# Optimization experiments

Measured on AMD Instinct MI355X. Metric: run time of the kernel, lower is better.

Reference implementation:

```python
import jax, jax.numpy as jnp
import numpy as np

N_GROUPS = 32
N_HEADS = 16
EPS = 1e-5


def group_norm(x, w, b):
    # x: [B, C, T]
    B, C, T = x.shape
    xg = x.reshape(B, N_GROUPS, C // N_GROUPS, T)
    mu = xg.mean(axis=(2, 3), keepdims=True)
    var = xg.var(axis=(2, 3), keepdims=True)
    xn = ((xg - mu) * jax.lax.rsqrt(var + EPS)).reshape(B, C, T)
    return xn * w[None, :, None] + b[None, :, None]


def setup_inputs() -> dict:
    key = jax.random.key(0)
    ks = jax.random.split(key, 5)
    B, C, T = 4, 1024, 1024
    return {
        "x": jax.random.normal(ks[0], (B, C, T), jnp.float32),
        "norm_weight": jnp.ones((C,), jnp.float32),
        "norm_bias": jnp.zeros((C,), jnp.float32),
        "qkv_w": jax.random.normal(ks[1], (3 * C, C), jnp.float32) * 0.02,
        "qkv_b": jax.random.normal(ks[2], (3 * C,), jnp.float32) * 0.02,
        "proj_w": jax.random.normal(ks[3], (C, C), jnp.float32) * 0.02,
        "proj_b": jax.random.normal(ks[4], (C,), jnp.float32) * 0.02,
    }


def reference(x, norm_weight, norm_bias, qkv_w, qkv_b, proj_w, proj_b):
    B, C, T = x.shape
    H = N_HEADS
    ch = C // H
    # GroupNorm + 1x1 conv to QKV: [B, 3C, T]
    xn = group_norm(x, norm_weight, norm_bias)
    qkv = jnp.einsum('oc,bct->bot', qkv_w, xn) + qkv_b[None, :, None]
    # Legacy layout: [B, H*3*ch, T] -> [B, H, 3, ch, T]
    qkv = qkv.reshape(B, H, 3, ch, T)
    q, k, v = qkv[:, :, 0], qkv[:, :, 1], qkv[:, :, 2]
    scale = 1.0 / jnp.sqrt(jnp.sqrt(jnp.asarray(ch, x.dtype)))
    w = jnp.einsum('bhct,bhcs->bhts', q * scale, k * scale)
    w = jax.nn.softmax(w.astype(jnp.float32), axis=-1).astype(w.dtype)
    a = jnp.einsum('bhts,bhcs->bhct', w, v).reshape(B, C, T)
    h = jnp.einsum('oc,bct->bot', proj_w, a) + proj_b[None, :, None]
    return x + h
```

## Files before the change

### kernel.cpp

```cpp
#include <hip/hip_runtime.h>
#include <hip/hip_bf16.h>

typedef __bf16 bf16;
typedef bf16  bf16x4 __attribute__((ext_vector_type(4)));
typedef bf16  bf16x8 __attribute__((ext_vector_type(8)));
typedef float f32x4  __attribute__((ext_vector_type(4)));

union B8 { bf16x8 v; bf16 e[8]; };
union B4 { bf16x4 v; bf16 e[4]; };
union F4 { f32x4 v; float e[4]; };

#define GLOAD_LDS16(g, l)                                            \
  __builtin_amdgcn_global_load_lds(                                  \
      (const __attribute__((address_space(1))) void*)(g),            \
      (__attribute__((address_space(3))) void*)(l), 16, 0, 0)

#define SWZ(arr, R, c8) (*(const bf16x8*)&(arr)[(size_t)(R) * 64 + (((c8) ^ ((R) & 7)) << 3)])

__global__ __launch_bounds__(256) void conv_w_kernel(
    const float* __restrict__ qkvw, const float* __restrict__ qkvb,
    const float* __restrict__ pw,
    bf16* __restrict__ Wb, bf16* __restrict__ Pb, float* __restrict__ bs)
{
  const int row = blockIdx.x;
  const int tid = threadIdx.x;
  if (row < 3072) {
    const float s = ((row % 192) < 128) ? 0.42468158f : 1.0f;
    const float4 a = ((const float4*)(qkvw + (size_t)row * 1024))[tid];
    B4 o;
    o.e[0] = (bf16)(a.x * s); o.e[1] = (bf16)(a.y * s);
    o.e[2] = (bf16)(a.z * s); o.e[3] = (bf16)(a.w * s);
    ((bf16x4*)(Wb + (size_t)row * 1024))[tid] = o.v;
    if (tid == 0) bs[row] = qkvb[row] * s;
  } else {
    const int r = row - 3072;
    const float4 a = ((const float4*)(pw + (size_t)r * 1024))[tid];
    B4 o;
    o.e[0] = (bf16)a.x; o.e[1] = (bf16)a.y;
    o.e[2] = (bf16)a.z; o.e[3] = (bf16)a.w;
    ((bf16x4*)(Pb + (size_t)r * 1024))[tid] = o.v;
  }
}

__global__ __launch_bounds__(256) void gn_t_kernel(
    const float* __restrict__ x, const float* __restrict__ w,
    const float* __restrict__ bias, bf16* __restrict__ xnt)
{
  const int blk = blockIdx.x;
  const int b = blk >> 5, g = blk & 31;
  const float* xp = x + (size_t)(b * 1024 + g * 32) * 1024;
  const int tid = threadIdx.x;

  float s = 0.f, ss = 0.f;
  for (int ch = tid; ch < 4096; ch += 256) {
    const float4* p = (const float4*)(xp + (size_t)ch * 8);
    float4 u0 = p[0], u1 = p[1];
    s  += u0.x + u0.y + u0.z + u0.w + u1.x + u1.y + u1.z + u1.w;
    ss += u0.x*u0.x + u0.y*u0.y + u0.z*u0.z + u0.w*u0.w
        + u1.x*u1.x + u1.y*u1.y + u1.z*u1.z + u1.w*u1.w;
  }
  #pragma unroll
  for (int m = 1; m < 64; m <<= 1) { s += __shfl_xor(s, m); ss += __shfl_xor(ss, m); }

  __shared__ float red[8];
  __shared__ float stats[2];
  const int wave = tid >> 6, lane = tid & 63;
  if (lane == 0) { red[wave] = s; red[4 + wave] = ss; }
  __syncthreads();
  if (tid == 0) {
    float ts  = red[0] + red[1] + red[2] + red[3];
    float tss = red[4] + red[5] + red[6] + red[7];
    float mu  = ts * (1.f / 32768.f);
    float var = tss * (1.f / 32768.f) - mu * mu;
    stats[0] = mu;
    stats[1] = rsqrtf(var + 1e-5f);
  }
  __syncthreads();
  const float mu = stats[0], rs = stats[1];

  for (int ti = 0; ti < 4; ++ti) {
    const int t = ti * 256 + tid;
    B8 o[4];
    #pragma unroll
    for (int cc = 0; cc < 32; ++cc) {
      const float wt = w[g * 32 + cc] * rs;
      const float bsv = bias[g * 32 + cc];
      const float v = xp[(size_t)cc * 1024 + t];
      o[cc >> 3].e[cc & 7] = (bf16)((v - mu) * wt + bsv);
    }
    bf16* dst = xnt + (size_t)(b * 1024 + t) * 1024 + g * 32;
    #pragma unroll
    for (int j = 0; j < 4; ++j) *(bf16x8*)(dst + j * 8) = o[j].v;
  }
}

__global__ __launch_bounds__(512, 2) void gemm_qkv_kernel(
    const bf16* __restrict__ xnt, const bf16* __restrict__ Wb,
    const float* __restrict__ bs, bf16* __restrict__ qkT, bf16* __restrict__ vv)
{
  const int bid = blockIdx.x;
  const int swz = (bid & 7) * 32 + (bid >> 3);
  const int bxn = swz >> 4, bym = swz & 15;
  const int n0 = bxn * 192, m0 = bym * 256;
  const int head = bxn;

  __shared__ __align__(16) bf16 Al[2][256 * 64];
  __shared__ __align__(16) bf16 Bl[2][192 * 64];

  const int tid  = threadIdx.x;
  const int wave = tid >> 6, lane = tid & 63;
  const int quad = lane >> 4, l15 = lane & 15;
  const int wr = wave >> 2, wc = wave & 3;
  const int lrow = lane >> 3, lp = lane & 7;
  const int sc8 = (lp ^ lrow) << 3;

  #define STAGE(bufn, kt) do {                                                \
    _Pragma("unroll")                                                         \
    for (int c = 0; c < 4; ++c)                                               \
      GLOAD_LDS16(xnt + (size_t)(m0 + c * 64 + wave * 8 + lrow) * 1024 +      \
                      (size_t)(kt) * 64 + sc8,                                \
                  &Al[bufn][(c * 64 + wave * 8) * 64]);                       \
    _Pragma("unroll")                                                         \
    for (int c = 0; c < 3; ++c)                                               \
      GLOAD_LDS16(Wb + (size_t)(n0 + c * 64 + wave * 8 + lrow) * 1024 +       \
                      (size_t)(kt) * 64 + sc8,                                \
                  &Bl[bufn][(c * 64 + wave * 8) * 64]);                       \
  } while (0)

  F4 acc[8][3];
  #pragma unroll
  for (int i = 0; i < 8; ++i)
    #pragma unroll
    for (int j = 0; j < 3; ++j) acc[i][j].v = (f32x4){0.f, 0.f, 0.f, 0.f};

  STAGE(0, 0);
  __syncthreads();

  for (int t = 0; t < 16; ++t) {
    const int cb = t & 1;

    bf16x8 af[2][8], bfr[2][3];
    #pragma unroll
    for (int kk = 0; kk < 2; ++kk) {
      #pragma unroll
      for (int nt = 0; nt < 3; ++nt)
        bfr[kk][nt] = SWZ(Bl[cb], wc * 48 + nt * 16 + l15, kk * 4 + quad);
      #pragma unroll
      for (int mt = 0; mt < 8; ++mt)
        af[kk][mt] = SWZ(Al[cb], wr * 128 + mt * 16 + l15, kk * 4 + quad);
    }

    if (t + 1 < 16) STAGE(cb ^ 1, t + 1);

    #pragma unroll
    for (int kk = 0; kk < 2; ++kk)
      #pragma unroll
      for (int mt = 0; mt < 8; ++mt)
        #pragma unroll
        for (int nt = 0; nt < 3; ++nt)
          acc[mt][nt].v = __builtin_amdgcn_mfma_f32_16x16x32_bf16(
              af[kk][mt], bfr[kk][nt], acc[mt][nt].v, 0, 0, 0);

    __syncthreads();
  }
  #undef STAGE

  const int z  = m0 >> 10;
  const int tb = (m0 & 1023) + wr * 128;
  #pragma unroll
  for (int nt = 0; nt < 3; ++nt) {
    const int r192 = wc * 48 + nt * 16;
    const float bb = bs[n0 + r192 + l15];
    if (r192 < 128) {
      const int col = head * 128 + r192 + l15;
      #pragma unroll
      for (int mt = 0; mt < 8; ++mt)
        #pragma unroll
        for (int r = 0; r < 4; ++r) {
          const int m = m0 + wr * 128 + mt * 16 + quad * 4 + r;
          qkT[(size_t)m * 2048 + col] = (bf16)(acc[mt][nt].e[r] + bb);
        }
    } else {
      bf16* vrow = vv + ((size_t)z * 1024 + head * 64 + (r192 - 128) + l15) * 1024;
      #pragma unroll
      for (int mt = 0; mt < 8; ++mt) {
        B4 pk;
        #pragma unroll
        for (int r = 0; r < 4; ++r) pk.e[r] = (bf16)(acc[mt][nt].e[r] + bb);
        *(bf16x4*)&vrow[tb + mt * 16 + quad * 4] = pk.v;
      }
    }
  }
}

__global__ __launch_bounds__(256) void gemm_proj_kernel(
    const bf16* __restrict__ Pb, const bf16* __restrict__ Bt,
    float* __restrict__ Cf, const float* __restrict__ bias,
    const float* __restrict__ resf)
{
  const int z = blockIdx.z;
  Bt   += (size_t)z * 1024 * 1024;
  Cf   += (size_t)z * 1024 * 1024;
  resf += (size_t)z * 1024 * 1024;
  const int n0 = blockIdx.x * 64, m0 = blockIdx.y * 64;

  __shared__ __align__(16) bf16 Al[64 * 64];
  __shared__ __align__(16) bf16 Bl[64 * 64];

  const int tid  = threadIdx.x;
  const int wave = tid >> 6, lane = tid & 63;
  const int quad = lane >> 4, l15 = lane & 15;
  const int wr = wave >> 1, wc = wave & 1;
  const int lrow = lane >> 3, lp = lane & 7;

  F4 acc[2][2];
  #pragma unroll
  for (int i = 0; i < 2; ++i)
    #pragma unroll
    for (int j = 0; j < 2; ++j) acc[i][j].v = (f32x4){0.f, 0.f, 0.f, 0.f};

  for (int k0 = 0; k0 < 1024; k0 += 64) {
    #pragma unroll
    for (int call = 0; call < 2; ++call) {
      const int row = wave * 16 + call * 8 + lrow;
      const int c8  = lp ^ (row & 7);
      GLOAD_LDS16(Pb + (size_t)(m0 + row) * 1024 + k0 + c8 * 8,
                  &Al[(wave * 16 + call * 8) * 64]);
      GLOAD_LDS16(Bt + (size_t)(n0 + row) * 1024 + k0 + c8 * 8,
                  &Bl[(wave * 16 + call * 8) * 64]);
    }
    __syncthreads();

    #pragma unroll
    for (int ks = 0; ks < 2; ++ks) {
      bf16x8 af[2], bfr[2];
      #pragma unroll
      for (int mt = 0; mt < 2; ++mt)
        af[mt] = SWZ(Al, wr * 32 + mt * 16 + l15, ks * 4 + quad);
      #pragma unroll
      for (int nt = 0; nt < 2; ++nt)
        bfr[nt] = SWZ(Bl, wc * 32 + nt * 16 + l15, ks * 4 + quad);
      #pragma unroll
      for (int mt = 0; mt < 2; ++mt)
        #pragma unroll
        for (int nt = 0; nt < 2; ++nt)
          acc[mt][nt].v = __builtin_amdgcn_mfma_f32_16x16x32_bf16(
              af[mt], bfr[nt], acc[mt][nt].v, 0, 0, 0);
    }
    __syncthreads();
  }

  #pragma unroll
  for (int mt = 0; mt < 2; ++mt) {
    #pragma unroll
    for (int r = 0; r < 4; ++r) {
      const int m = m0 + wr * 32 + mt * 16 + quad * 4 + r;
      const float bb = bias[m];
      #pragma unroll
      for (int nt = 0; nt < 2; ++nt) {
        const int n = n0 + wc * 32 + nt * 16 + l15;
        Cf[(size_t)m * 1024 + n] = acc[mt][nt].e[r] + bb + resf[(size_t)m * 1024 + n];
      }
    }
  }
}

__global__ __launch_bounds__(256) void attn_kernel(
    const bf16* __restrict__ qkTin, const bf16* __restrict__ vmat,
    bf16* __restrict__ aout)
{
  const int h = blockIdx.x, tt = blockIdx.y, z = blockIdx.z;
  const bf16* qk = qkTin + (size_t)z * 1024 * 2048;
  const bf16* vp = vmat + (size_t)z * 1024 * 1024 + (size_t)(h * 64) * 1024;
  aout += (size_t)z * 1024 * 1024;
  const int t0 = tt * 128;

  __shared__ __align__(16) bf16 qP[128 * 64];
  __shared__ __align__(16) bf16 kl[2][64 * 64];
  __shared__ __align__(16) bf16 vl[2][64 * 64];

  const int tid  = threadIdx.x;
  const int wave = tid >> 6, lane = tid & 63;
  const int quad = lane >> 4, l15 = lane & 15;
  const int lrow = lane >> 3, lp = lane & 7;

  #pragma unroll
  for (int c = 0; c < 4; ++c) {
    const int row = wave * 32 + c * 8 + lrow;
    const int c8  = lp ^ (row & 7);
    GLOAD_LDS16(qk + (size_t)(t0 + row) * 2048 + h * 128 + c8 * 8,
                &qP[(wave * 32 + c * 8) * 64]);
  }
  const int r0 = wave * 16 + lrow, r1 = wave * 16 + 8 + lrow;
  const int c80 = lp ^ (r0 & 7), c81 = lp ^ (r1 & 7);
  GLOAD_LDS16(qk + (size_t)r0 * 2048 + h * 128 + 64 + c80 * 8, &kl[0][(wave * 16) * 64]);
  GLOAD_LDS16(qk + (size_t)r1 * 2048 + h * 128 + 64 + c81 * 8, &kl[0][(wave * 16 + 8) * 64]);
  GLOAD_LDS16(vp + (size_t)r0 * 1024 + c80 * 8, &vl[0][(wave * 16) * 64]);
  GLOAD_LDS16(vp + (size_t)r1 * 1024 + c81 * 8, &vl[0][(wave * 16 + 8) * 64]);
  __syncthreads();

  bf16x8 bq0[2], bq1[2];
  int prow[2];
  #pragma unroll
  for (int b = 0; b < 2; ++b) {
    const int Rq = wave * 32 + b * 16 + l15;
    bq0[b] = SWZ(qP, Rq, quad);
    bq1[b] = SWZ(qP, Rq, quad + 4);
    prow[b] = Rq;
  }

  float l_i[2] = {0.f, 0.f};
  F4 oacc[2][4];
  #pragma unroll
  for (int b = 0; b < 2; ++b)
    #pragma unroll
    for (int ct = 0; ct < 4; ++ct) oacc[b][ct].v = (f32x4){0.f, 0.f, 0.f, 0.f};

  const int pq8 = (quad & 1) * 4;

  int buf = 0;
  for (int s0 = 0; s0 < 1024; s0 += 64) {
    if (s0 + 64 < 1024) {
      const int nb = buf ^ 1, sn = s0 + 64;
      GLOAD_LDS16(qk + (size_t)(sn + r0) * 2048 + h * 128 + 64 + c80 * 8,
                  &kl[nb][(wave * 16) * 64]);
      GLOAD_LDS16(qk + (size_t)(sn + r1) * 2048 + h * 128 + 64 + c81 * 8,
                  &kl[nb][(wave * 16 + 8) * 64]);
      GLOAD_LDS16(vp + (size_t)r0 * 1024 + sn + c80 * 8, &vl[nb][(wave * 16) * 64]);
      GLOAD_LDS16(vp + (size_t)r1 * 1024 + sn + c81 * 8, &vl[nb][(wave * 16 + 8) * 64]);
    }

    bf16x8 ak0[4], ak1[4], bv[2][4];
    #pragma unroll
    for (int st = 0; st < 4; ++st) {
      const int Rk = st * 16 + l15;
      ak0[st] = SWZ(kl[buf], Rk, quad);
      ak1[st] = SWZ(kl[buf], Rk, quad + 4);
    }
    #pragma unroll
    for (int ks = 0; ks < 2; ++ks)
      #pragma unroll
      for (int ct = 0; ct < 4; ++ct)
        bv[ks][ct] = SWZ(vl[buf], ct * 16 + l15, ks * 4 + quad);

    #pragma unroll
    for (int b = 0; b < 2; ++b) {
      F4 sacc[4];
      #pragma unroll
      for (int st = 0; st < 4; ++st) sacc[st].v = (f32x4){0.f, 0.f, 0.f, 0.f};
      #pragma unroll
      for (int st = 0; st < 4; ++st) {
        sacc[st].v = __builtin_amdgcn_mfma_f32_16x16x32_bf16(ak0[st], bq0[b], sacc[st].v, 0, 0, 0);
        sacc[st].v = __builtin_amdgcn_mfma_f32_16x16x32_bf16(ak1[st], bq1[b], sacc[st].v, 0, 0, 0);
      }

      bf16* const pbase = &qP[(size_t)prow[b] * 64];
      #pragma unroll
      for (int st = 0; st < 4; ++st) {
        B4 pk;
        #pragma unroll
        for (int r = 0; r < 4; ++r) {
          const float p = __builtin_amdgcn_exp2f(sacc[st].e[r]);
          l_i[b] += p;
          pk.e[r] = (bf16)p;
        }
        const int c8 = (st * 2 + (quad >> 1)) ^ (prow[b] & 7);
        *(bf16x4*)(pbase + (c8 << 3) + pq8) = pk.v;
      }

      #pragma unroll
      for (int ks = 0; ks < 2; ++ks) {
        const bf16x8 ap = SWZ(qP, prow[b], ks * 4 + quad);
        #pragma unroll
        for (int ct = 0; ct < 4; ++ct)
          oacc[b][ct].v = __builtin_amdgcn_mfma_f32_16x16x32_bf16(
              ap, bv[ks][ct], oacc[b][ct].v, 0, 0, 0);
      }
    }
    __syncthreads();
    buf ^= 1;
  }

  #pragma unroll
  for (int b = 0; b < 2; ++b) {
    float li = l_i[b];
    li += __shfl_xor(li, 16);
    li += __shfl_xor(li, 32);
    const float inv = 1.f / li;
    float iv[4];
    #pragma unroll
    for (int r = 0; r < 4; ++r) iv[r] = __shfl(inv, quad * 4 + r);
    #pragma unroll
    for (int r = 0; r < 4; ++r) {
      const int t = t0 + wave * 32 + b * 16 + quad * 4 + r;
      #pragma unroll
      for (int ct = 0; ct < 4; ++ct)
        aout[(size_t)t * 1024 + h * 64 + ct * 16 + l15] = (bf16)(oacc[b][ct].e[r] * iv[r]);
    }
  }
}

extern "C" void kernel_launch(void* const* d_in, const int* in_sizes, int n_in,
                              void* d_out, int out_size, void* d_ws, size_t ws_size,
                              hipStream_t stream)
{
  const float* x    = (const float*)d_in[0];
  const float* nw   = (const float*)d_in[1];
  const float* nb   = (const float*)d_in[2];
  const float* qkvw = (const float*)d_in[3];
  const float* qkvb = (const float*)d_in[4];
  const float* pw   = (const float*)d_in[5];
  const float* pb   = (const float*)d_in[6];
  float* out = (float*)d_out;

  const long M1 = 1024L * 1024L;
  bf16*  xnt = (bf16*)d_ws;
  bf16*  qkT = xnt + 4 * M1;
  bf16*  vv  = xnt + 12 * M1;
  bf16*  at  = xnt + 16 * M1;
  bf16*  Wb  = xnt + 20 * M1;
  bf16*  Pb  = xnt + 23 * M1;
  float* bs  = (float*)(xnt + 24 * M1);

  conv_w_kernel<<<dim3(4096), dim3(256), 0, stream>>>(qkvw, qkvb, pw, Wb, Pb, bs);
  gn_t_kernel<<<dim3(128), dim3(256), 0, stream>>>(x, nw, nb, xnt);
  gemm_qkv_kernel<<<dim3(256), dim3(512), 0, stream>>>(xnt, Wb, bs, qkT, vv);
  attn_kernel<<<dim3(16, 8, 4), dim3(256), 0, stream>>>(qkT, vv, at);
  gemm_proj_kernel<<<dim3(16, 16, 4), dim3(256), 0, stream>>>(Pb, at, out, pb, x);
}
```

Baseline: 176.1 us.

## Retile proj GEMM to 128x128 double-buffered tiles and split GroupNorm blocks

The projection GEMM moves from 64x64 tiles with 256 threads and a 3D grid to 128x128 tiles with 512 threads, a flat 256-block grid with a block-index swizzle, and double-buffered LDS. The next K-tile's global-to-LDS loads are issued before the current MFMAs, so load latency overlaps compute and operand reuse per block rises. The GroupNorm kernel now uses two blocks per group, each writing half of the T range, doubling the block count for more parallelism. The cost is that each half-block recomputes the full group statistics, and the GEMM uses more LDS and registers per block, which can lower occupancy.

```diff
diff --git a/kernel.cpp b/kernel.cpp
--- a/kernel.cpp
+++ b/kernel.cpp
@@ -47,7 +47,7 @@
     const float* __restrict__ bias, bf16* __restrict__ xnt)
 {
   const int blk = blockIdx.x;
-  const int b = blk >> 5, g = blk & 31;
+  const int b = blk >> 6, g = (blk >> 1) & 31, half = blk & 1;
   const float* xp = x + (size_t)(b * 1024 + g * 32) * 1024;
   const int tid = threadIdx.x;
 
@@ -78,7 +78,7 @@
   __syncthreads();
   const float mu = stats[0], rs = stats[1];
 
-  for (int ti = 0; ti < 4; ++ti) {
+  for (int ti = half * 2; ti < half * 2 + 2; ++ti) {
     const int t = ti * 256 + tid;
     B8 o[4];
     #pragma unroll
@@ -193,73 +193,92 @@
   }
 }
 
-__global__ __launch_bounds__(256) void gemm_proj_kernel(
+__global__ __launch_bounds__(512, 2) void gemm_proj_kernel(
     const bf16* __restrict__ Pb, const bf16* __restrict__ Bt,
-    float* __restrict__ Cf, const float* __restrict__ bias,
+    float* __restrict__ out, const float* __restrict__ bias,
     const float* __restrict__ resf)
 {
-  const int z = blockIdx.z;
-  Bt   += (size_t)z * 1024 * 1024;
-  Cf   += (size_t)z * 1024 * 1024;
-  resf += (size_t)z * 1024 * 1024;
-  const int n0 = blockIdx.x * 64, m0 = blockIdx.y * 64;
-
-  __shared__ __align__(16) bf16 Al[64 * 64];
-  __shared__ __align__(16) bf16 Bl[64 * 64];
+  const int bid = blockIdx.x;
+  const int swz = (bid & 7) * 32 + (bid >> 3);
+  const int mp = swz & 7, np = swz >> 3;
+  const int m0 = mp * 128;
+  const int n0g = np * 128;
+
+  __shared__ __align__(16) bf16 Al[2][128 * 64];
+  __shared__ __align__(16) bf16 Bl[2][128 * 64];
 
   const int tid  = threadIdx.x;
   const int wave = tid >> 6, lane = tid & 63;
   const int quad = lane >> 4, l15 = lane & 15;
-  const int wr = wave >> 1, wc = wave & 1;
+  const int wr = wave >> 2, wc = wave & 3;
   const int lrow = lane >> 3, lp = lane & 7;
-
-  F4 acc[2][2];
-  #pragma unroll
-  for (int i = 0; i < 2; ++i)
+  const int sc8 = (lp ^ lrow) << 3;
+
+  #define STAGE(bufn, kt) do {                                                \
+    _Pragma("unroll")                                                         \
+    for (int c = 0; c < 2; ++c)                                               \
+      GLOAD_LDS16(Pb + (size_t)(m0 + c * 64 + wave * 8 + lrow) * 1024 +       \
+                      (size_t)(kt) * 64 + sc8,                                \
+                  &Al[bufn][(c * 64 + wave * 8) * 64]);                       \
+    _Pragma("unroll")                                                         \
+    for (int c = 0; c < 2; ++c)                                               \
+      GLOAD_LDS16(Bt + (size_t)(n0g + c * 64 + wave * 8 + lrow) * 1024 +      \
+                      (size_t)(kt) * 64 + sc8,                                \
+                  &Bl[bufn][(c * 64 + wave * 8) * 64]);                       \
+  } while (0)
+
+  F4 acc[4][2];
+  #pragma unroll
+  for (int i = 0; i < 4; ++i)
     #pragma unroll
     for (int j = 0; j < 2; ++j) acc[i][j].v = (f32x4){0.f, 0.f, 0.f, 0.f};
 
-  for (int k0 = 0; k0 < 1024; k0 += 64) {
-    #pragma unroll
-    for (int call = 0; call < 2; ++call) {
-      const int row = wave * 16 + call * 8 + lrow;
-      const int c8  = lp ^ (row & 7);
-      GLOAD_LDS16(Pb + (size_t)(m0 + row) * 1024 + k0 + c8 * 8,
-                  &Al[(wave * 16 + call * 8) * 64]);
-      GLOAD_LDS16(Bt + (size_t)(n0 + row) * 1024 + k0 + c8 * 8,
-                  &Bl[(wave * 16 + call * 8) * 64]);
-    }
-    __syncthreads();
-
-    #pragma unroll
-    for (int ks = 0; ks < 2; ++ks) {
-      bf16x8 af[2], bfr[2];
-      #pragma unroll
-      for (int mt = 0; mt < 2; ++mt)
-        af[mt] = SWZ(Al, wr * 32 + mt * 16 + l15, ks * 4 + quad);
+  STAGE(0, 0);
+  __syncthreads();
+
+  for (int t = 0; t < 16; ++t) {
+    const int cb = t & 1;
+
+    bf16x8 af[2][4], bfr[2][2];
+    #pragma unroll
+    for (int kk = 0; kk < 2; ++kk) {
+      #pragma unroll
+      for (int mt = 0; mt < 4; ++mt)
+        af[kk][mt] = SWZ(Al[cb], wr * 64 + mt * 16 + l15, kk * 4 + quad);
       #pragma unroll
       for (int nt = 0; nt < 2; ++nt)
-        bfr[nt] = SWZ(Bl, wc * 32 + nt * 16 + l15, ks * 4 + quad);
-      #pragma unroll
-      for (int mt = 0; mt < 2; ++mt)
+        bfr[kk][nt] = SWZ(Bl[cb], wc * 32 + nt * 16 + l15, kk * 4 + quad);
+    }
+
+    if (t + 1 < 16) STAGE(cb ^ 1, t + 1);
+
+    #pragma unroll
+    for (int kk = 0; kk < 2; ++kk)
+      #pragma unroll
+      for (int mt = 0; mt < 4; ++mt)
         #pragma unroll
         for (int nt = 0; nt < 2; ++nt)
           acc[mt][nt].v = __builtin_amdgcn_mfma_f32_16x16x32_bf16(
-              af[mt], bfr[nt], acc[mt][nt].v, 0, 0, 0);
-    }
+              af[kk][mt], bfr[kk][nt], acc[mt][nt].v, 0, 0, 0);
+
     __syncthreads();
   }
-
-  #pragma unroll
-  for (int mt = 0; mt < 2; ++mt) {
+  #undef STAGE
+
+  const int z  = n0g >> 10;
+  const int nl = n0g & 1023;
+  const size_t zoff = (size_t)z * 1024 * 1024;
+  #pragma unroll
+  for (int mt = 0; mt < 4; ++mt) {
     #pragma unroll
     for (int r = 0; r < 4; ++r) {
-      const int m = m0 + wr * 32 + mt * 16 + quad * 4 + r;
+      const int m = m0 + wr * 64 + mt * 16 + quad * 4 + r;
       const float bb = bias[m];
       #pragma unroll
       for (int nt = 0; nt < 2; ++nt) {
-        const int n = n0 + wc * 32 + nt * 16 + l15;
-        Cf[(size_t)m * 1024 + n] = acc[mt][nt].e[r] + bb + resf[(size_t)m * 1024 + n];
+        const int n = nl + wc * 32 + nt * 16 + l15;
+        out[zoff + (size_t)m * 1024 + n] =
+            acc[mt][nt].e[r] + bb + resf[zoff + (size_t)m * 1024 + n];
       }
     }
   }
@@ -423,8 +442,8 @@
   float* bs  = (float*)(xnt + 24 * M1);
 
   conv_w_kernel<<<dim3(4096), dim3(256), 0, stream>>>(qkvw, qkvb, pw, Wb, Pb, bs);
-  gn_t_kernel<<<dim3(128), dim3(256), 0, stream>>>(x, nw, nb, xnt);
+  gn_t_kernel<<<dim3(256), dim3(256), 0, stream>>>(x, nw, nb, xnt);
   gemm_qkv_kernel<<<dim3(256), dim3(512), 0, stream>>>(xnt, Wb, bs, qkT, vv);
   attn_kernel<<<dim3(16, 8, 4), dim3(256), 0, stream>>>(qkT, vv, at);
-  gemm_proj_kernel<<<dim3(16, 16, 4), dim3(256), 0, stream>>>(Pb, at, out, pb, x);
-}
+  gemm_proj_kernel<<<dim3(256), dim3(512), 0, stream>>>(Pb, at, out, pb, x);
+}
```

After: 180.9 us. 1.03x slower.
